# Performance work log

Measured on AMD Instinct MI355X. Metric: run time of the kernel, lower is better.

The kernel has to match this reference:

```python
import jax, jax.numpy as jnp
import numpy as np

N = 50000   # nodes
E = 800000  # edges
D = 200     # h_dim == out_dim
R = 500     # num_rels
L = 2       # num_hidden_layers
RRELU_SLOPE = (1.0 / 8.0 + 1.0 / 3.0) / 2.0  # eval-mode F.rrelu negative slope


def _rrelu(x):
    return jnp.where(x >= 0, x, x * jnp.float32(RRELU_SLOPE))


def setup_inputs() -> dict:
    key = jax.random.key(0)
    ks = jax.random.split(key, 10)
    s = np.float32(1.0 / np.sqrt(D))  # ~xavier scale
    return {
        "init_ent_emb": jax.random.normal(ks[0], (N, D), jnp.float32),
        "rel_emb": jax.random.normal(ks[1], (R, D), jnp.float32),
        "weight_neighbor": jax.random.normal(ks[2], (L, D, D), jnp.float32) * s,
        "loop_weight": jax.random.normal(ks[3], (L, D, D), jnp.float32) * s,
        "evolve_loop_weight": jax.random.normal(ks[4], (L, D, D), jnp.float32) * s,
        "norm": jax.random.uniform(ks[5], (N, 1), jnp.float32),
        "src": jax.random.randint(ks[6], (E,), 0, N, dtype=jnp.int32),
        "dst": jax.random.randint(ks[7], (E,), 0, N, dtype=jnp.int32),
        "etype": jax.random.randint(ks[8], (E,), 0, R, dtype=jnp.int32),
        "node_id": jnp.arange(N, dtype=jnp.int32),
    }


def reference(init_ent_emb, rel_emb, weight_neighbor, loop_weight,
              evolve_loop_weight, norm, src, dst, etype, node_id):
    # g.ndata['h'] = init_ent_emb[node_id]
    h = init_ent_emb[node_id]                                    # [N, D]
    # mask of nodes with in-degree > 0 (fixed across layers)
    indeg = jnp.zeros((N,), jnp.float32).at[dst].add(1.0)
    has_in = (indeg > 0)[:, None]                                # [N, 1]
    for l in range(L):
        # loop message: loop_weight where in-degree>0, evolve_loop_weight otherwise
        loop_msg = jnp.where(has_in,
                             h @ loop_weight[l],
                             h @ evolve_loop_weight[l])          # [N, D]
        # per-edge message: (h_src + rel_emb[etype]) @ W_neighbor
        msg = (h[src] + rel_emb[etype]) @ weight_neighbor[l]     # [E, D]
        # sum-scatter to destination nodes, then per-node norm (apply_func)
        agg = jax.ops.segment_sum(msg, dst, num_segments=N)      # [N, D]
        h = _rrelu(agg * norm + loop_msg)
    return h
```

## Files before the change

kernel.cpp:

```cpp
#include <hip/hip_runtime.h>

#define D 200
#define RRELU_SLOPE 0.22916666666666666f
#define STRIDE 96

typedef unsigned short u16;
typedef unsigned int u32;

using bf16x8 = __attribute__((ext_vector_type(8))) short;
using f32x4  = __attribute__((ext_vector_type(4))) float;

__device__ __forceinline__ float rrelu(float x) {
    return x >= 0.0f ? x : x * RRELU_SLOPE;
}
__device__ __forceinline__ float bf2f(u32 u) {
    union { u32 i; float f; } c; c.i = u << 16; return c.f;
}
__device__ __forceinline__ u32 f2bf(float f) {
    union { float f; u32 i; } c; c.f = f;
    return (c.i + 0x7fffu + ((c.i >> 16) & 1u)) >> 16;
}
__device__ __forceinline__ void gll16(const void* g, void* l) {
    __builtin_amdgcn_global_load_lds((const __attribute__((address_space(1))) void*)g,
                                     (__attribute__((address_space(3))) void*)l,
                                     16, 0, 0);
}


__global__ void fill_k(u32* __restrict__ ep, u32 dummy, int n4) {
    int i = blockIdx.x * blockDim.x + threadIdx.x;
    if (i < n4) {
        uint4 v = {dummy, dummy, dummy, dummy};
        *(uint4*)(ep + (size_t)i * 4) = v;
    }
}

__global__ void scatter_k(const int* __restrict__ dst, const int* __restrict__ src,
                          const int* __restrict__ etype, int* __restrict__ cnt,
                          u32* __restrict__ ep, int E) {
    int e = blockIdx.x * blockDim.x + threadIdx.x;
    if (e < E) {
        int d = dst[e];
        int c = atomicAdd(&cnt[d], 1);
        if (c < STRIDE)
            ep[(size_t)d * STRIDE + c] = (u32)src[e] | ((u32)etype[e] << 17);
    }
}

__global__ void noin_k(const int* __restrict__ cnt, int* __restrict__ noin,
                       int* __restrict__ noin_cnt, int N) {
    int v = blockIdx.x * blockDim.x + threadIdx.x;
    if (v < N && cnt[v] == 0) noin[atomicAdd(noin_cnt, 1)] = v;
}


__global__ void gather_k(const float* __restrict__ init, const int* __restrict__ nid,
                         u16* __restrict__ hb, int N) {
    int lane = threadIdx.x & 63;
    int v = blockIdx.x * 4 + (threadIdx.x >> 6);
    if (v >= N || lane >= 50) return;
    float4 f = *(const float4*)(init + (size_t)nid[v] * D + lane * 4);
    uint2 o;
    o.x = f2bf(f.x) | (f2bf(f.y) << 16);
    o.y = f2bf(f.z) | (f2bf(f.w) << 16);
    *(uint2*)(hb + (size_t)v * D + lane * 4) = o;
}


__global__ void relb_k(const float* __restrict__ rel, u16* __restrict__ relb, int n) {
    int i = blockIdx.x * blockDim.x + threadIdx.x;
    if (i < n) relb[i] = (u16)f2bf(rel[i]);
}

__global__ void bt_k(const float* __restrict__ Wn, const float* __restrict__ Wl,
                     u16* __restrict__ Bt) {
    int idx = blockIdx.x * blockDim.x + threadIdx.x;
    if (idx >= 2 * 256 * 416) return;
    int l = idx / (256 * 416);
    int rem = idx % (256 * 416);
    int c = rem / 416;
    int k = rem % 416;
    float v = 0.0f;
    if (c < 200 && k < 400)
        v = (k < 200) ? Wn[(size_t)l * 40000 + k * 200 + c]
                      : Wl[(size_t)l * 40000 + (k - 200) * 200 + c];
    Bt[idx] = (u16)f2bf(v);
}

#define ACC8(q, z0, z1, z2, z3) { z0 += bf2f(q.x & 0xffffu); z1 += bf2f(q.x >> 16); \
                                  z2 += bf2f(q.y & 0xffffu); z3 += bf2f(q.y >> 16); }


__global__ void gagg0_k(const u16* __restrict__ hb, const u16* __restrict__ relb,
                        const u32* __restrict__ ep, const int* __restrict__ cnt,
                        const float* __restrict__ norm,
                        u16* __restrict__ aggb, u16* __restrict__ relsumb, int N) {
    int lane = threadIdx.x & 63;
    int v = blockIdx.x * 4 + (threadIdx.x >> 6);
    if (v >= N || lane >= 50) return;
    int beg = v * STRIDE;
    int end = beg + ((cnt[v] + 15) & ~15);
    size_t lo = (size_t)lane * 4;
    float a0 = 0, a1 = 0, a2 = 0, a3 = 0;
    float r0 = 0, r1 = 0, r2 = 0, r3 = 0;
    for (int i = beg; i < end; i += 16) {
        u32 p[16];
#pragma unroll
        for (int j = 0; j < 16; ++j) p[j] = ep[i + j];
        uint2 qh[16], qr[16];
#pragma unroll
        for (int j = 0; j < 16; ++j)
            qh[j] = *(const uint2*)(hb + (size_t)(p[j] & 0x1FFFF) * D + lo);
#pragma unroll
        for (int j = 0; j < 16; ++j)
            qr[j] = *(const uint2*)(relb + (size_t)((p[j] >> 17) & 0x3FF) * D + lo);
#pragma unroll
        for (int j = 0; j < 16; ++j) {
            ACC8(qh[j], a0, a1, a2, a3);
            ACC8(qr[j], r0, r1, r2, r3);
        }
    }
    uint2 rs;
    rs.x = f2bf(r0) | (f2bf(r1) << 16);
    rs.y = f2bf(r2) | (f2bf(r3) << 16);
    *(uint2*)(relsumb + (size_t)v * D + lo) = rs;
    float nv = norm[v];
    uint2 o;
    o.x = f2bf((a0 + r0) * nv) | (f2bf((a1 + r1) * nv) << 16);
    o.y = f2bf((a2 + r2) * nv) | (f2bf((a3 + r3) * nv) << 16);
    *(uint2*)(aggb + (size_t)v * D + lo) = o;
}


__global__ void gagg1_k(const u16* __restrict__ hb, const u32* __restrict__ ep,
                        const int* __restrict__ cnt, const float* __restrict__ norm,
                        const u16* __restrict__ addb, u16* __restrict__ outb, int N) {
    int lane = threadIdx.x & 63;
    int v = blockIdx.x * 4 + (threadIdx.x >> 6);
    if (v >= N || lane >= 50) return;
    int beg = v * STRIDE;
    int end = beg + ((cnt[v] + 15) & ~15);
    size_t lo = (size_t)lane * 4;
    float a0 = 0, a1 = 0, a2 = 0, a3 = 0;
    for (int i = beg; i < end; i += 16) {
        u32 p[16];
#pragma unroll
        for (int j = 0; j < 16; ++j) p[j] = ep[i + j];
        uint2 q[16];
#pragma unroll
        for (int j = 0; j < 16; ++j)
            q[j] = *(const uint2*)(hb + (size_t)(p[j] & 0x1FFFF) * D + lo);
#pragma unroll
        for (int j = 0; j < 16; ++j) ACC8(q[j], a0, a1, a2, a3);
    }
    {
        uint2 q = *(const uint2*)(addb + (size_t)v * D + lo);
        ACC8(q, a0, a1, a2, a3);
    }
    float nv = norm[v];
    uint2 o;
    o.x = f2bf(a0 * nv) | (f2bf(a1 * nv) << 16);
    o.y = f2bf(a2 * nv) | (f2bf(a3 * nv) << 16);
    *(uint2*)(outb + (size_t)v * D + lo) = o;
}


__global__ __launch_bounds__(256) void gemm_k(
        const u16* __restrict__ Aagg, const u16* __restrict__ Ah,
        const u16* __restrict__ Bt,
        float* __restrict__ outF, u16* __restrict__ outB, int M) {
    __shared__ __align__(16) u16 As[128 * 32];
    __shared__ __align__(16) u16 Bs[64 * 32];
    int tid = threadIdx.x;
    int lane = tid & 63;
    int wave = tid >> 6;
    int rowBase = blockIdx.x * 128;
    int colBase = blockIdx.y * 64;
    int wr = (wave >> 1) * 64;
    int wc = (wave & 1) * 32;
    int m = lane & 15;
    int kq = (lane >> 4) * 8;

    int srow = tid >> 2;
    int kg = (tid & 3) * 8;

    u16* ldsA0 = As + ((size_t)(wave * 64) * 8);
    u16* ldsA1 = As + ((size_t)(256 + wave * 64) * 8);
    u16* ldsB  = Bs + ((size_t)(wave * 64) * 8);

    f32x4 acc[4][2] = {};

    for (int k0 = 0; k0 < 416; k0 += 32) {
        int k = k0 + kg;
        {
            const u16* g0 = (k < 200) ? Aagg + (size_t)(rowBase + srow) * D + k
                                      : Ah + (size_t)(rowBase + srow) * D + (k - 200);
            gll16(g0, ldsA0);
            const u16* g1 = (k < 200) ? Aagg + (size_t)(rowBase + srow + 64) * D + k
                                      : Ah + (size_t)(rowBase + srow + 64) * D + (k - 200);
            gll16(g1, ldsA1);
            const u16* gb = Bt + (size_t)(colBase + srow) * 416 + k;
            gll16(gb, ldsB);
        }
        __syncthreads();

        bf16x8 a0 = *(const bf16x8*)(As + (wr + m) * 32 + kq);
        bf16x8 a1 = *(const bf16x8*)(As + (wr + 16 + m) * 32 + kq);
        bf16x8 a2 = *(const bf16x8*)(As + (wr + 32 + m) * 32 + kq);
        bf16x8 a3 = *(const bf16x8*)(As + (wr + 48 + m) * 32 + kq);
        bf16x8 b0 = *(const bf16x8*)(Bs + (wc + m) * 32 + kq);
        bf16x8 b1 = *(const bf16x8*)(Bs + (wc + 16 + m) * 32 + kq);
        acc[0][0] = __builtin_amdgcn_mfma_f32_16x16x32_bf16(a0, b0, acc[0][0], 0, 0, 0);
        acc[0][1] = __builtin_amdgcn_mfma_f32_16x16x32_bf16(a0, b1, acc[0][1], 0, 0, 0);
        acc[1][0] = __builtin_amdgcn_mfma_f32_16x16x32_bf16(a1, b0, acc[1][0], 0, 0, 0);
        acc[1][1] = __builtin_amdgcn_mfma_f32_16x16x32_bf16(a1, b1, acc[1][1], 0, 0, 0);
        acc[2][0] = __builtin_amdgcn_mfma_f32_16x16x32_bf16(a2, b0, acc[2][0], 0, 0, 0);
        acc[2][1] = __builtin_amdgcn_mfma_f32_16x16x32_bf16(a2, b1, acc[2][1], 0, 0, 0);
        acc[3][0] = __builtin_amdgcn_mfma_f32_16x16x32_bf16(a3, b0, acc[3][0], 0, 0, 0);
        acc[3][1] = __builtin_amdgcn_mfma_f32_16x16x32_bf16(a3, b1, acc[3][1], 0, 0, 0);
        __syncthreads();
    }

    int cRow = (lane >> 4) * 4;
    int cCol = lane & 15;
#pragma unroll
    for (int i = 0; i < 4; ++i) {
#pragma unroll
        for (int j = 0; j < 2; ++j) {
            int col = colBase + wc + j * 16 + cCol;
            if (col >= 200) continue;
#pragma unroll
            for (int r = 0; r < 4; ++r) {
                int row = rowBase + wr + i * 16 + cRow + r;
                if (row < M) {
                    float val = rrelu(acc[i][j][r]);
                    if (outF) outF[(size_t)row * D + col] = val;
                    if (outB) outB[(size_t)row * D + col] = (u16)f2bf(val);
                }
            }
        }
    }
}


__global__ void fixup_k(const u16* __restrict__ hb, const float* __restrict__ We,
                        const int* __restrict__ noin, const int* __restrict__ noin_cnt,
                        float* __restrict__ outF, u16* __restrict__ outB) {
    int cnt = *noin_cnt;
    for (int i = blockIdx.x; i < cnt; i += gridDim.x) {
        int v = noin[i];
        int j = threadIdx.x;
        if (j < D) {
            float acc = 0.0f;
            for (int k = 0; k < D; ++k)
                acc += bf2f(hb[(size_t)v * D + k]) * We[(size_t)k * D + j];
            float r = rrelu(acc);
            if (outF) outF[(size_t)v * D + j] = r;
            if (outB) outB[(size_t)v * D + j] = (u16)f2bf(r);
        }
    }
}

extern "C" void kernel_launch(void* const* d_in, const int* in_sizes, int n_in,
                              void* d_out, int out_size, void* d_ws, size_t ws_size,
                              hipStream_t stream) {
    const float* init  = (const float*)d_in[0];
    const float* rel   = (const float*)d_in[1];
    const float* Wn    = (const float*)d_in[2];
    const float* Wl    = (const float*)d_in[3];
    const float* We    = (const float*)d_in[4];
    const float* norm  = (const float*)d_in[5];
    const int* src     = (const int*)d_in[6];
    const int* dst     = (const int*)d_in[7];
    const int* etype   = (const int*)d_in[8];
    const int* node_id = (const int*)d_in[9];
    float* out = (float*)d_out;

    int N = in_sizes[5];
    int E = in_sizes[6];
    size_t NP = (size_t)N + 256;

    char* w = (char*)d_ws;
    auto carve = [&](size_t bytes) {
        char* p = w;
        w += (bytes + 255) & ~(size_t)255;
        return p;
    };
    u16* hb0     = (u16*)carve(NP * D * sizeof(u16));
    u16* hb1     = (u16*)carve(NP * D * sizeof(u16));
    u16* aggb    = (u16*)carve(NP * D * sizeof(u16));
    u16* relsumb = (u16*)carve((size_t)N * D * sizeof(u16));
    u16* relb    = (u16*)carve((size_t)501 * D * sizeof(u16));
    u16* Bt      = (u16*)carve((size_t)2 * 256 * 416 * sizeof(u16));
    int* cnt     = (int*)carve((size_t)N * sizeof(int));
    u32* epack   = (u32*)carve((size_t)N * STRIDE * sizeof(u32));
    int* noin    = (int*)carve((size_t)N * sizeof(int));
    int* noin_cnt = (int*)carve(sizeof(int));

    hipMemsetAsync(cnt, 0, (size_t)N * sizeof(int), stream);
    hipMemsetAsync(noin_cnt, 0, sizeof(int), stream);
    hipMemsetAsync(hb0 + (size_t)N * D, 0, D * sizeof(u16), stream);
    hipMemsetAsync(hb1 + (size_t)N * D, 0, D * sizeof(u16), stream);
    hipMemsetAsync(relb + (size_t)500 * D, 0, D * sizeof(u16), stream);

    u32 dummy = (u32)N | (500u << 17);
    int n4 = (N * STRIDE) / 4;
    fill_k<<<(n4 + 255) / 256, 256, 0, stream>>>(epack, dummy, n4);
    scatter_k<<<(E + 255) / 256, 256, 0, stream>>>(dst, src, etype, cnt, epack, E);
    noin_k<<<(N + 255) / 256, 256, 0, stream>>>(cnt, noin, noin_cnt, N);

    gather_k<<<(N + 3) / 4, 256, 0, stream>>>(init, node_id, hb0, N);
    relb_k<<<(500 * D + 255) / 256, 256, 0, stream>>>(rel, relb, 500 * D);
    bt_k<<<(2 * 256 * 416 + 255) / 256, 256, 0, stream>>>(Wn, Wl, Bt);

    dim3 gg((N + 127) / 128, 4);

    gagg0_k<<<(N + 3) / 4, 256, 0, stream>>>(hb0, relb, epack, cnt, norm,
                                             aggb, relsumb, N);
    gemm_k<<<gg, 256, 0, stream>>>(aggb, hb0, Bt, nullptr, hb1, N);
    fixup_k<<<8, 256, 0, stream>>>(hb0, We, noin, noin_cnt, nullptr, hb1);

    gagg1_k<<<(N + 3) / 4, 256, 0, stream>>>(hb1, epack, cnt, norm,
                                             relsumb, aggb, N);
    gemm_k<<<gg, 256, 0, stream>>>(aggb, hb1, Bt + 256 * 416, out, nullptr, N);
    fixup_k<<<8, 256, 0, stream>>>(hb1, We + D * D, noin, noin_cnt, out, nullptr);
}
```

Baseline: 408.1 us.

## Widen gather loads to 16 bytes, pad edge lists to 8, fuse prep kernels

The aggregation kernels now assign two nodes per wave, with 25 lanes each loading 16-byte chunks instead of 50 lanes loading 8-byte chunks. Edge padding drops from 16 to 8 entries, and only the padding slots are filled with the dummy index, which replaces the full fill of the edge-pack buffer. The relation, weight-transpose and dummy-row setup kernels plus several memsets are merged into one prep kernel. The aim is fewer load instructions, less wasted padding traffic and fewer kernel launches, at the cost of more idle lanes per wave (25 of 32 active).

```diff
diff --git a/kernel.cpp b/kernel.cpp
--- a/kernel.cpp
+++ b/kernel.cpp
@@ -3,6 +3,7 @@
 #define D 200
 #define RRELU_SLOPE 0.22916666666666666f
 #define STRIDE 96
+#define PAD 8
 
 typedef unsigned short u16;
 typedef unsigned int u32;
@@ -19,6 +20,9 @@
 __device__ __forceinline__ u32 f2bf(float f) {
     union { float f; u32 i; } c; c.f = f;
     return (c.i + 0x7fffu + ((c.i >> 16) & 1u)) >> 16;
+}
+__device__ __forceinline__ u32 pack2(float x, float y) {
+    return f2bf(x) | (f2bf(y) << 16);
 }
 __device__ __forceinline__ void gll16(const void* g, void* l) {
     __builtin_amdgcn_global_load_lds((const __attribute__((address_space(1))) void*)g,
@@ -26,14 +30,35 @@
                                      16, 0, 0);
 }
 
-
-__global__ void fill_k(u32* __restrict__ ep, u32 dummy, int n4) {
+__device__ __forceinline__ void accu4(uint4 q, float* acc) {
+    acc[0] += bf2f(q.x & 0xffffu); acc[1] += bf2f(q.x >> 16);
+    acc[2] += bf2f(q.y & 0xffffu); acc[3] += bf2f(q.y >> 16);
+    acc[4] += bf2f(q.z & 0xffffu); acc[5] += bf2f(q.z >> 16);
+    acc[6] += bf2f(q.w & 0xffffu); acc[7] += bf2f(q.w >> 16);
+}
+
+
+__global__ void prep_k(const float* __restrict__ rel, const float* __restrict__ Wn,
+                       const float* __restrict__ Wl, u16* __restrict__ relb,
+                       u16* __restrict__ Bt, u16* __restrict__ hb0d,
+                       u16* __restrict__ hb1d, int* __restrict__ noin_cnt) {
     int i = blockIdx.x * blockDim.x + threadIdx.x;
-    if (i < n4) {
-        uint4 v = {dummy, dummy, dummy, dummy};
-        *(uint4*)(ep + (size_t)i * 4) = v;
-    }
-}
+    if (i == 0) *noin_cnt = 0;
+    if (i < 200) { hb0d[i] = 0; hb1d[i] = 0; }
+    if (i < 100200) relb[i] = (i < 100000) ? (u16)f2bf(rel[i]) : (u16)0;
+    if (i < 2 * 256 * 416) {
+        int l = i / (256 * 416);
+        int rem = i % (256 * 416);
+        int c = rem / 416;
+        int k = rem % 416;
+        float v = 0.0f;
+        if (c < 200 && k < 400)
+            v = (k < 200) ? Wn[(size_t)l * 40000 + k * 200 + c]
+                          : Wl[(size_t)l * 40000 + (k - 200) * 200 + c];
+        Bt[i] = (u16)f2bf(v);
+    }
+}
+
 
 __global__ void scatter_k(const int* __restrict__ dst, const int* __restrict__ src,
                           const int* __restrict__ etype, int* __restrict__ cnt,
@@ -47,10 +72,14 @@
     }
 }
 
-__global__ void noin_k(const int* __restrict__ cnt, int* __restrict__ noin,
-                       int* __restrict__ noin_cnt, int N) {
+__global__ void pad_k(const int* __restrict__ cnt, u32* __restrict__ ep, u32 dummy,
+                      int* __restrict__ noin, int* __restrict__ noin_cnt, int N) {
     int v = blockIdx.x * blockDim.x + threadIdx.x;
-    if (v < N && cnt[v] == 0) noin[atomicAdd(noin_cnt, 1)] = v;
+    if (v >= N) return;
+    int c = cnt[v];
+    if (c == 0) noin[atomicAdd(noin_cnt, 1)] = v;
+    int e = (c + PAD - 1) & ~(PAD - 1);
+    for (int i = c; i < e; ++i) ep[(size_t)v * STRIDE + i] = dummy;
 }
 
 
@@ -61,34 +90,10 @@
     if (v >= N || lane >= 50) return;
     float4 f = *(const float4*)(init + (size_t)nid[v] * D + lane * 4);
     uint2 o;
-    o.x = f2bf(f.x) | (f2bf(f.y) << 16);
-    o.y = f2bf(f.z) | (f2bf(f.w) << 16);
+    o.x = pack2(f.x, f.y);
+    o.y = pack2(f.z, f.w);
     *(uint2*)(hb + (size_t)v * D + lane * 4) = o;
 }
-
-
-__global__ void relb_k(const float* __restrict__ rel, u16* __restrict__ relb, int n) {
-    int i = blockIdx.x * blockDim.x + threadIdx.x;
-    if (i < n) relb[i] = (u16)f2bf(rel[i]);
-}
-
-__global__ void bt_k(const float* __restrict__ Wn, const float* __restrict__ Wl,
-                     u16* __restrict__ Bt) {
-    int idx = blockIdx.x * blockDim.x + threadIdx.x;
-    if (idx >= 2 * 256 * 416) return;
-    int l = idx / (256 * 416);
-    int rem = idx % (256 * 416);
-    int c = rem / 416;
-    int k = rem % 416;
-    float v = 0.0f;
-    if (c < 200 && k < 400)
-        v = (k < 200) ? Wn[(size_t)l * 40000 + k * 200 + c]
-                      : Wl[(size_t)l * 40000 + (k - 200) * 200 + c];
-    Bt[idx] = (u16)f2bf(v);
-}
-
-#define ACC8(q, z0, z1, z2, z3) { z0 += bf2f(q.x & 0xffffu); z1 += bf2f(q.x >> 16); \
-                                  z2 += bf2f(q.y & 0xffffu); z3 += bf2f(q.y >> 16); }
 
 
 __global__ void gagg0_k(const u16* __restrict__ hb, const u16* __restrict__ relb,
@@ -96,39 +101,43 @@
                         const float* __restrict__ norm,
                         u16* __restrict__ aggb, u16* __restrict__ relsumb, int N) {
     int lane = threadIdx.x & 63;
-    int v = blockIdx.x * 4 + (threadIdx.x >> 6);
-    if (v >= N || lane >= 50) return;
+    int wave = threadIdx.x >> 6;
+    int li = lane & 31;
+    int v = blockIdx.x * 8 + wave * 2 + (lane >> 5);
+    if (v >= N || li >= 25) return;
+    size_t lo = (size_t)li * 8;
+    const u16* hbL = hb + lo;
+    const u16* rbL = relb + lo;
+    int c = cnt[v];
+    int rv = (c + PAD - 1) >> 3;
     int beg = v * STRIDE;
-    int end = beg + ((cnt[v] + 15) & ~15);
-    size_t lo = (size_t)lane * 4;
-    float a0 = 0, a1 = 0, a2 = 0, a3 = 0;
-    float r0 = 0, r1 = 0, r2 = 0, r3 = 0;
-    for (int i = beg; i < end; i += 16) {
-        u32 p[16];
-#pragma unroll
-        for (int j = 0; j < 16; ++j) p[j] = ep[i + j];
-        uint2 qh[16], qr[16];
-#pragma unroll
-        for (int j = 0; j < 16; ++j)
-            qh[j] = *(const uint2*)(hb + (size_t)(p[j] & 0x1FFFF) * D + lo);
-#pragma unroll
-        for (int j = 0; j < 16; ++j)
-            qr[j] = *(const uint2*)(relb + (size_t)((p[j] >> 17) & 0x3FF) * D + lo);
-#pragma unroll
-        for (int j = 0; j < 16; ++j) {
-            ACC8(qh[j], a0, a1, a2, a3);
-            ACC8(qr[j], r0, r1, r2, r3);
-        }
-    }
-    uint2 rs;
-    rs.x = f2bf(r0) | (f2bf(r1) << 16);
-    rs.y = f2bf(r2) | (f2bf(r3) << 16);
-    *(uint2*)(relsumb + (size_t)v * D + lo) = rs;
+    float a[8] = {}, rr[8] = {};
+    for (int r = 0; r < rv; ++r) {
+        int ib = beg + r * PAD;
+        u32 p[8];
+#pragma unroll
+        for (int j = 0; j < 8; ++j) p[j] = ep[ib + j];
+        uint4 qh[8], qr[8];
+#pragma unroll
+        for (int j = 0; j < 8; ++j)
+            qh[j] = *(const uint4*)(hbL + (size_t)(p[j] & 0x1FFFF) * D);
+#pragma unroll
+        for (int j = 0; j < 8; ++j)
+            qr[j] = *(const uint4*)(rbL + (size_t)((p[j] >> 17) & 0x3FF) * D);
+#pragma unroll
+        for (int j = 0; j < 8; ++j) { accu4(qh[j], a); accu4(qr[j], rr); }
+    }
+    uint4 rs;
+    rs.x = pack2(rr[0], rr[1]); rs.y = pack2(rr[2], rr[3]);
+    rs.z = pack2(rr[4], rr[5]); rs.w = pack2(rr[6], rr[7]);
+    *(uint4*)(relsumb + (size_t)v * D + lo) = rs;
     float nv = norm[v];
-    uint2 o;
-    o.x = f2bf((a0 + r0) * nv) | (f2bf((a1 + r1) * nv) << 16);
-    o.y = f2bf((a2 + r2) * nv) | (f2bf((a3 + r3) * nv) << 16);
-    *(uint2*)(aggb + (size_t)v * D + lo) = o;
+    uint4 o;
+    o.x = pack2((a[0] + rr[0]) * nv, (a[1] + rr[1]) * nv);
+    o.y = pack2((a[2] + rr[2]) * nv, (a[3] + rr[3]) * nv);
+    o.z = pack2((a[4] + rr[4]) * nv, (a[5] + rr[5]) * nv);
+    o.w = pack2((a[6] + rr[6]) * nv, (a[7] + rr[7]) * nv);
+    *(uint4*)(aggb + (size_t)v * D + lo) = o;
 }
 
 
@@ -136,32 +145,39 @@
                         const int* __restrict__ cnt, const float* __restrict__ norm,
                         const u16* __restrict__ addb, u16* __restrict__ outb, int N) {
     int lane = threadIdx.x & 63;
-    int v = blockIdx.x * 4 + (threadIdx.x >> 6);
-    if (v >= N || lane >= 50) return;
+    int wave = threadIdx.x >> 6;
+    int li = lane & 31;
+    int v = blockIdx.x * 8 + wave * 2 + (lane >> 5);
+    if (v >= N || li >= 25) return;
+    size_t lo = (size_t)li * 8;
+    const u16* hbL = hb + lo;
+    int c = cnt[v];
+    int rv = (c + PAD - 1) >> 3;
     int beg = v * STRIDE;
-    int end = beg + ((cnt[v] + 15) & ~15);
-    size_t lo = (size_t)lane * 4;
-    float a0 = 0, a1 = 0, a2 = 0, a3 = 0;
-    for (int i = beg; i < end; i += 16) {
-        u32 p[16];
-#pragma unroll
-        for (int j = 0; j < 16; ++j) p[j] = ep[i + j];
-        uint2 q[16];
-#pragma unroll
-        for (int j = 0; j < 16; ++j)
-            q[j] = *(const uint2*)(hb + (size_t)(p[j] & 0x1FFFF) * D + lo);
-#pragma unroll
-        for (int j = 0; j < 16; ++j) ACC8(q[j], a0, a1, a2, a3);
+    float a[8] = {};
+    for (int r = 0; r < rv; ++r) {
+        int ib = beg + r * PAD;
+        u32 p[8];
+#pragma unroll
+        for (int j = 0; j < 8; ++j) p[j] = ep[ib + j];
+        uint4 q[8];
+#pragma unroll
+        for (int j = 0; j < 8; ++j)
+            q[j] = *(const uint4*)(hbL + (size_t)(p[j] & 0x1FFFF) * D);
+#pragma unroll
+        for (int j = 0; j < 8; ++j) accu4(q[j], a);
     }
     {
-        uint2 q = *(const uint2*)(addb + (size_t)v * D + lo);
-        ACC8(q, a0, a1, a2, a3);
+        uint4 q = *(const uint4*)(addb + (size_t)v * D + lo);
+        accu4(q, a);
     }
     float nv = norm[v];
-    uint2 o;
-    o.x = f2bf(a0 * nv) | (f2bf(a1 * nv) << 16);
-    o.y = f2bf(a2 * nv) | (f2bf(a3 * nv) << 16);
-    *(uint2*)(outb + (size_t)v * D + lo) = o;
+    uint4 o;
+    o.x = pack2(a[0] * nv, a[1] * nv);
+    o.y = pack2(a[2] * nv, a[3] * nv);
+    o.z = pack2(a[4] * nv, a[5] * nv);
+    o.w = pack2(a[6] * nv, a[7] * nv);
+    *(uint4*)(outb + (size_t)v * D + lo) = o;
 }
 
 
@@ -297,30 +313,25 @@
     int* noin    = (int*)carve((size_t)N * sizeof(int));
     int* noin_cnt = (int*)carve(sizeof(int));
 
-    hipMemsetAsync(cnt, 0, (size_t)N * sizeof(int), stream);
-    hipMemsetAsync(noin_cnt, 0, sizeof(int), stream);
-    hipMemsetAsync(hb0 + (size_t)N * D, 0, D * sizeof(u16), stream);
-    hipMemsetAsync(hb1 + (size_t)N * D, 0, D * sizeof(u16), stream);
-    hipMemsetAsync(relb + (size_t)500 * D, 0, D * sizeof(u16), stream);
-
+    (void)hipMemsetAsync(cnt, 0, (size_t)N * sizeof(int), stream);
+
+    int prepN = 2 * 256 * 416;
+    prep_k<<<(prepN + 255) / 256, 256, 0, stream>>>(rel, Wn, Wl, relb, Bt,
+                                                    hb0 + (size_t)N * D,
+                                                    hb1 + (size_t)N * D, noin_cnt);
+    scatter_k<<<(E + 255) / 256, 256, 0, stream>>>(dst, src, etype, cnt, epack, E);
     u32 dummy = (u32)N | (500u << 17);
-    int n4 = (N * STRIDE) / 4;
-    fill_k<<<(n4 + 255) / 256, 256, 0, stream>>>(epack, dummy, n4);
-    scatter_k<<<(E + 255) / 256, 256, 0, stream>>>(dst, src, etype, cnt, epack, E);
-    noin_k<<<(N + 255) / 256, 256, 0, stream>>>(cnt, noin, noin_cnt, N);
-
+    pad_k<<<(N + 255) / 256, 256, 0, stream>>>(cnt, epack, dummy, noin, noin_cnt, N);
     gather_k<<<(N + 3) / 4, 256, 0, stream>>>(init, node_id, hb0, N);
-    relb_k<<<(500 * D + 255) / 256, 256, 0, stream>>>(rel, relb, 500 * D);
-    bt_k<<<(2 * 256 * 416 + 255) / 256, 256, 0, stream>>>(Wn, Wl, Bt);
 
     dim3 gg((N + 127) / 128, 4);
 
-    gagg0_k<<<(N + 3) / 4, 256, 0, stream>>>(hb0, relb, epack, cnt, norm,
+    gagg0_k<<<(N + 7) / 8, 256, 0, stream>>>(hb0, relb, epack, cnt, norm,
                                              aggb, relsumb, N);
     gemm_k<<<gg, 256, 0, stream>>>(aggb, hb0, Bt, nullptr, hb1, N);
     fixup_k<<<8, 256, 0, stream>>>(hb0, We, noin, noin_cnt, nullptr, hb1);
 
-    gagg1_k<<<(N + 3) / 4, 256, 0, stream>>>(hb1, epack, cnt, norm,
+    gagg1_k<<<(N + 7) / 8, 256, 0, stream>>>(hb1, epack, cnt, norm,
                                              relsumb, aggb, N);
     gemm_k<<<gg, 256, 0, stream>>>(aggb, hb1, Bt + 256 * 416, out, nullptr, N);
     fixup_k<<<8, 256, 0, stream>>>(hb1, We + D * D, noin, noin_cnt, out, nullptr);
```

After: 371.1 us. 9.1% less time.
